# Optimization experiments

Hardware: AMD Instinct MI355X
Metric: run time of the kernel (lower is better)

## Reference

```python
import jax, jax.numpy as jnp
import numpy as np

D_K = 32
TOPK_FRAC = 0.1
DROP_P = 0.1


def setup_inputs() -> dict:
    key = jax.random.key(0)
    k1, k2, k3, k4 = jax.random.split(key, 4)
    B, F, N, T = 4, 64, 4096, 12
    dim = T * F  # 768
    x = jax.random.normal(k1, (B, F, N, T), dtype=jnp.float32)
    # nn.Linear(dim, d_k, bias=False): y = x @ W.T ; store W transposed as [dim, d_k]
    W_Q = jax.random.normal(k2, (dim, D_K), dtype=jnp.float32) * (1.0 / np.sqrt(dim))
    W_K = jax.random.normal(k3, (dim, D_K), dtype=jnp.float32) * (1.0 / np.sqrt(dim))
    # uniform noise driving F.dropout (training=True) deterministically
    drop_u = jax.random.uniform(k4, (N, N), dtype=jnp.float32)
    return {"x": x, "W_Q": W_Q, "W_K": W_K, "drop_u": drop_u}


def _drop(attn, drop_u):
    # k = int(N*N*0.1); topk over flattened matrix
    N, M = attn.shape
    k = int(N * M * TOPK_FRAC)
    flat = attn.reshape(-1)
    _, idx = jax.lax.top_k(flat, k)
    topk_mask = jnp.zeros_like(flat).at[idx].set(1.0).reshape(N, M)
    kept = attn * topk_mask
    # F.dropout on the remainder: zero with prob p, scale survivors by 1/(1-p)
    keep = (drop_u >= DROP_P).astype(attn.dtype)
    remaining = attn * (1.0 - topk_mask) * keep * (1.0 / (1.0 - DROP_P))
    return kept + remaining


def reference(x, W_Q, W_K, drop_u):
    B, F, N, T = x.shape
    # [B, F, N, T] -> [B, N, T, F] -> [B, N, T*F]
    xr = jnp.transpose(x, (0, 2, 3, 1)).reshape(B, N, T * F)
    Q = xr @ W_Q  # [B, N, d_k]
    K = xr @ W_K  # [B, N, d_k]
    scores = jnp.einsum("bnd,bmd->bnm", Q, K) * (1.0 / np.sqrt(D_K))  # [B, N, N]
    attn = jax.nn.softmax(jnp.sum(scores, axis=0), axis=-1)  # [N, N]
    return _drop(attn, drop_u)
```

## Files before the change

kernel.cpp:

```cpp
#include <hip/hip_runtime.h>
#include <stdint.h>

#define NN 4096
#define KSEL_S 419430u
#define INV_SQRT_DK 0.17677669529663687f

#define OFF_QH 0u
#define OFF_KH (1u<<20)
#define OFF_STATS (2u<<20)
#define OFF_H   (3u<<20)
#define OFF_H2  (4u<<20)
#define OFF_ST  ((4u<<20) + 65536u)
#define OFF_MASK (5u<<20)
#define OFF_SB  (16u<<20)
#define WS_NEED_B16 (48u<<20)

#define LDB 104

typedef __attribute__((ext_vector_type(8))) short bf16x8;
typedef __attribute__((ext_vector_type(8))) unsigned short u16x8;
typedef __attribute__((ext_vector_type(4))) float f32x4;

static __device__ __forceinline__ short f2bf(float f) {
    unsigned u = __float_as_uint(f);
    unsigned r = (u + 0x7FFFu + ((u >> 16) & 1u)) >> 16;
    return (short)r;
}
static __device__ __forceinline__ float bf2f(short h) {
    return __uint_as_float(((unsigned)(unsigned short)h) << 16);
}

__global__ __launch_bounds__(256) void projmask_kernel(
    const float* __restrict__ x, const float* __restrict__ WQ,
    const float* __restrict__ WK,
    short* __restrict__ Qh, short* __restrict__ Kh,
    const float4* __restrict__ u4, unsigned* __restrict__ maskw)
{
    __shared__ short Ah[2][64 * LDB];
    __shared__ short Al[2][64 * LDB];
    __shared__ short Bl[2][64 * LDB];
    const int bxg = blockIdx.x;
    const int tid = threadIdx.x;

    if (bxg >= 256) {
        const unsigned word = (unsigned)(bxg - 256) * 256 + tid;
        const float4* __restrict__ up = u4 + (size_t)word * 8;
        unsigned m = 0;
#pragma unroll
        for (int j = 0; j < 8; ++j) {
            float4 a = up[j];
            m |= (a.x >= 0.1f ? 1u : 0u) << (4 * j);
            m |= (a.y >= 0.1f ? 2u : 0u) << (4 * j);
            m |= (a.z >= 0.1f ? 4u : 0u) << (4 * j);
            m |= (a.w >= 0.1f ? 8u : 0u) << (4 * j);
        }
        maskw[word] = m;
        return;
    }

    const int bx  = bxg;
    const int b   = bx >> 6;
    const int n0  = (bx & 63) << 6;
    const int l   = tid & 63;
    const int w   = __builtin_amdgcn_readfirstlane(tid >> 6);
    const int lr  = l & 15;
    const int kg  = (l >> 4) * 8;

    f32x4 acc[4];
#pragma unroll
    for (int j = 0; j < 4; ++j) acc[j] = (f32x4){0.f, 0.f, 0.f, 0.f};

    auto STAGE = [&](int c, int sbuf) {
#pragma unroll
        for (int j = 0; j < 6; ++j) {
            const int s   = tid + (j << 8);
            const int f_l = s / 192;
            const int rem = s - f_l * 192;
            const int r   = rem / 3;
            const int t4  = rem - r * 3;
            float4 v = *(const float4*)(x + (size_t)b * 3145728
                                          + (size_t)(c * 8 + f_l) * 49152
                                          + (size_t)(n0 + r) * 12 + t4 * 4);
            const int kl = f_l * 12 + t4 * 4;
            short4 hi, lo;
            hi.x = f2bf(v.x); lo.x = f2bf(v.x - bf2f(hi.x));
            hi.y = f2bf(v.y); lo.y = f2bf(v.y - bf2f(hi.y));
            hi.z = f2bf(v.z); lo.z = f2bf(v.z - bf2f(hi.z));
            hi.w = f2bf(v.w); lo.w = f2bf(v.w - bf2f(hi.w));
            *(short4*)&Ah[sbuf][r * LDB + kl] = hi;
            *(short4*)&Al[sbuf][r * LDB + kl] = lo;
        }
#pragma unroll
        for (int j = 0; j < 6; ++j) {
            const int s   = tid + (j << 8);
            const int qk  = (s >= 768) ? 1 : 0;
            const int rem = s - qk * 768;
            const int kr  = rem >> 3;
            const int c4  = rem & 7;
            const int t   = kr % 12;
            const int f_l = kr / 12;
            const float* __restrict__ Wp = qk ? WK : WQ;
            float4 wv = *(const float4*)(Wp + (size_t)(t * 64 + c * 8 + f_l) * 32 + (c4 << 2));
            const int kl = f_l * 12 + t;
            const int col = (qk << 5) + (c4 << 2);
            Bl[sbuf][(col + 0) * LDB + kl] = f2bf(wv.x);
            Bl[sbuf][(col + 1) * LDB + kl] = f2bf(wv.y);
            Bl[sbuf][(col + 2) * LDB + kl] = f2bf(wv.z);
            Bl[sbuf][(col + 3) * LDB + kl] = f2bf(wv.w);
        }
    };

    STAGE(0, 0);
    int buf = 0;
    for (int c = 0; c < 8; ++c) {
        __syncthreads();
        if (c < 7) STAGE(c + 1, buf ^ 1);
#pragma unroll
        for (int ks = 0; ks < 3; ++ks) {
            const int ko = ks * 32 + kg;
            bf16x8 ah = *(const bf16x8*)&Ah[buf][(w * 16 + lr) * LDB + ko];
            bf16x8 al = *(const bf16x8*)&Al[buf][(w * 16 + lr) * LDB + ko];
#pragma unroll
            for (int j = 0; j < 4; ++j) {
                bf16x8 bb = *(const bf16x8*)&Bl[buf][(j * 16 + lr) * LDB + ko];
                acc[j] = __builtin_amdgcn_mfma_f32_16x16x32_bf16(ah, bb, acc[j], 0, 0, 0);
                acc[j] = __builtin_amdgcn_mfma_f32_16x16x32_bf16(al, bb, acc[j], 0, 0, 0);
            }
        }
        buf ^= 1;
    }

#pragma unroll
    for (int j = 0; j < 4; ++j) {
        const int col = j * 16 + lr;
#pragma unroll
        for (int r = 0; r < 4; ++r) {
            const int row = n0 + w * 16 + (l >> 4) * 4 + r;
            if (col < 32)
                Qh[(size_t)row * 128 + (b << 5) + col] = f2bf(acc[j][r] * INV_SQRT_DK);
            else
                Kh[(size_t)row * 128 + (b << 5) + (col - 32)] = f2bf(acc[j][r]);
        }
    }
}

template<bool B16>
__global__ __launch_bounds__(256, 3) void gemm_kernel(
    const short* __restrict__ Qh, const short* __restrict__ Kh, void* Sv)
{
    const int bi = blockIdx.x >> 5, bj = blockIdx.x & 31;
    const int tid = threadIdx.x;
    const int w = tid >> 6, l = tid & 63;
    const int m0 = bi * 128 + (w >> 1) * 64;
    const int n0 = bj * 128 + (w & 1) * 64;
    const int lr = l & 15;
    const int kg = (l >> 4) * 8;

    f32x4 acc[4][4];
#pragma unroll
    for (int i = 0; i < 4; ++i)
#pragma unroll
        for (int j = 0; j < 4; ++j) acc[i][j] = (f32x4){0.f, 0.f, 0.f, 0.f};

    bf16x8 aA[4], bA[4], aB[4], bB[4];

    auto LD = [&](bf16x8* A, bf16x8* B, int k0) {
#pragma unroll
        for (int i = 0; i < 4; ++i) {
            A[i] = *(const bf16x8*)(Qh + (size_t)(m0 + i * 16 + lr) * 128 + k0 + kg);
            B[i] = *(const bf16x8*)(Kh + (size_t)(n0 + i * 16 + lr) * 128 + k0 + kg);
        }
    };
    auto DOMFMA = [&](bf16x8* A, bf16x8* B) {
#pragma unroll
        for (int i = 0; i < 4; ++i)
#pragma unroll
            for (int j = 0; j < 4; ++j)
                acc[i][j] = __builtin_amdgcn_mfma_f32_16x16x32_bf16(A[i], B[j], acc[i][j], 0, 0, 0);
    };

    LD(aA, bA, 0);
    LD(aB, bB, 32);
    DOMFMA(aA, bA);  LD(aA, bA, 64);
    DOMFMA(aB, bB);  LD(aB, bB, 96);
    DOMFMA(aA, bA);
    DOMFMA(aB, bB);

#pragma unroll
    for (int i = 0; i < 4; ++i) {
        int rowb = m0 + i * 16 + (l >> 4) * 4;
#pragma unroll
        for (int j = 0; j < 4; ++j) {
            int col = n0 + j * 16 + (l & 15);
#pragma unroll
            for (int r = 0; r < 4; ++r) {
                if constexpr (B16)
                    ((unsigned short*)Sv)[(size_t)(rowb + r) * NN + col] =
                        (unsigned short)f2bf(acc[i][j][r]);
                else
                    ((float*)Sv)[(size_t)(rowb + r) * NN + col] = acc[i][j][r];
            }
        }
    }
}

template<bool B16>
__global__ __launch_bounds__(512) void histstat_kernel(
    const void* __restrict__ Sv, float2* __restrict__ stats,
    unsigned* __restrict__ gh)
{
    __shared__ unsigned h[1024];
    const int tid = threadIdx.x;
    const int l = tid & 63;
    const int w = tid >> 6;

    for (int i = tid; i < 1024; i += 512) h[i] = 0;
    __syncthreads();

#pragma unroll
    for (int r = 0; r < 2; ++r) {
        const int row = (blockIdx.x << 4) + (r << 3) + w;

        float v[64];
        if constexpr (B16) {
            const u16x8* rp = (const u16x8*)((const unsigned short*)Sv + (size_t)row * NN);
#pragma unroll
            for (int j = 0; j < 8; ++j) {
                u16x8 e = rp[l + (j << 6)];
#pragma unroll
                for (int i = 0; i < 8; ++i) v[j * 8 + i] = bf2f((short)e[i]);
            }
        } else {
            const float4* rp = (const float4*)((const float*)Sv + (size_t)row * NN);
#pragma unroll
            for (int j = 0; j < 16; ++j) {
                float4 t = rp[l + (j << 6)];
                v[j * 4 + 0] = t.x; v[j * 4 + 1] = t.y;
                v[j * 4 + 2] = t.z; v[j * 4 + 3] = t.w;
            }
        }

        float s = 0.f;
#pragma unroll
        for (int j = 0; j < 64; ++j) { v[j] = __expf(v[j]); s += v[j]; }
#pragma unroll
        for (int off = 32; off; off >>= 1) s += __shfl_xor(s, off);
        const float inv = 1.0f / s;
        if (l == 0) stats[row] = make_float2(0.f, inv);

        if constexpr (B16) {
#pragma unroll
            for (int jj = 0; jj < 2; ++jj) {
                const int base = jj * 32;
#pragma unroll
                for (int c = 0; c < 8; ++c) {
                    int b0 = min(max((int)(__float_as_uint(v[base + c] * inv) >> 16) - 0x3780, 0), 1023);
                    atomicAdd(&h[b0], 1u);
                }
            }
        } else {
#pragma unroll
            for (int jj = 0; jj < 4; ++jj) {
                const int base = jj * 16;
#pragma unroll
                for (int c = 0; c < 4; ++c) {
                    int b0 = min(max((int)(__float_as_uint(v[base + c] * inv) >> 16) - 0x3780, 0), 1023);
                    atomicAdd(&h[b0], 1u);
                }
            }
        }
    }

    __syncthreads();
    unsigned* dst = gh + ((unsigned)blockIdx.x << 10);
    for (int i = tid; i < 1024; i += 512) dst[i] = h[i];
}

__global__ __launch_bounds__(1024) void reduce_kernel(
    const unsigned* __restrict__ gh, unsigned* __restrict__ gh2)
{
    const int t = threadIdx.x, b = blockIdx.x;
    unsigned s = 0;
    for (int p = 0; p < 32; ++p) s += gh[((unsigned)(b * 32 + p) << 10) + t];
    gh2[((unsigned)b << 10) + t] = s;
}

__global__ __launch_bounds__(1024) void scan_kernel(
    const unsigned* __restrict__ gh2, unsigned* st)
{
    __shared__ unsigned P[1024];
    const int t = threadIdx.x;
    unsigned s = 0;
#pragma unroll
    for (int p = 0; p < 8; ++p) s += gh2[(p << 10) + t];
    P[t] = s;
    __syncthreads();
    for (int off = 1; off < 1024; off <<= 1) {
        unsigned v = P[t] + ((t + off < 1024) ? P[t + off] : 0u);
        __syncthreads();
        P[t] = v;
        __syncthreads();
    }
    if (P[t] >= KSEL_S && (t == 1023 || P[t + 1] < KSEL_S))
        st[2] = (0x3780u + (unsigned)t) << 16;
}

template<bool B16>
__global__ __launch_bounds__(256) void final_kernel(
    const void* __restrict__ Sv, float* __restrict__ out,
    const unsigned* __restrict__ maskw,
    const float2* __restrict__ stats, const unsigned* __restrict__ st)
{
    const int row = blockIdx.x;
    const int tid = threadIdx.x;
    const float thr = __uint_as_float(st[2]);
    const float2 stt = stats[row];
    float4* o4 = (float4*)(out + (size_t)row * NN);
    const unsigned* mw = maskw + (size_t)row * 128;

    float4 sv[4];
    unsigned wv[4];

    if constexpr (B16) {
        const ushort4* S4 = (const ushort4*)((const unsigned short*)Sv + (size_t)row * NN);
        ushort4 sraw[4];
#pragma unroll
        for (int j = 0; j < 4; ++j) sraw[j] = S4[tid + (j << 8)];
#pragma unroll
        for (int j = 0; j < 4; ++j) wv[j] = mw[(tid >> 3) + (j << 5)];
#pragma unroll
        for (int j = 0; j < 4; ++j) {
            sv[j].x = bf2f((short)sraw[j].x); sv[j].y = bf2f((short)sraw[j].y);
            sv[j].z = bf2f((short)sraw[j].z); sv[j].w = bf2f((short)sraw[j].w);
        }
    } else {
        const float4* S4 = (const float4*)((const float*)Sv + (size_t)row * NN);
#pragma unroll
        for (int j = 0; j < 4; ++j) sv[j] = S4[tid + (j << 8)];
#pragma unroll
        for (int j = 0; j < 4; ++j) wv[j] = mw[(tid >> 3) + (j << 5)];
    }

    const unsigned sh = (tid & 7) << 2;
#pragma unroll
    for (int j = 0; j < 4; ++j) {
        const unsigned bits = (wv[j] >> sh) & 0xFu;
        float4 o;
        float p;
        p = __expf(sv[j].x - stt.x) * stt.y;
        o.x = (p >= thr) ? p : ((bits & 1u) ? p * (1.0f / 0.9f) : 0.0f);
        p = __expf(sv[j].y - stt.x) * stt.y;
        o.y = (p >= thr) ? p : ((bits & 2u) ? p * (1.0f / 0.9f) : 0.0f);
        p = __expf(sv[j].z - stt.x) * stt.y;
        o.z = (p >= thr) ? p : ((bits & 4u) ? p * (1.0f / 0.9f) : 0.0f);
        p = __expf(sv[j].w - stt.x) * stt.y;
        o.w = (p >= thr) ? p : ((bits & 8u) ? p * (1.0f / 0.9f) : 0.0f);
        o4[tid + (j << 8)] = o;
    }
}

extern "C" void kernel_launch(void* const* d_in, const int* in_sizes, int n_in,
                              void* d_out, int out_size, void* d_ws, size_t ws_size,
                              hipStream_t stream)
{
    const float* x  = (const float*)d_in[0];
    const float* WQ = (const float*)d_in[1];
    const float* WK = (const float*)d_in[2];
    const float* du = (const float*)d_in[3];
    float* out = (float*)d_out;
    char* ws = (char*)d_ws;

    short* Qh = (short*)(ws + OFF_QH);
    short* Kh = (short*)(ws + OFF_KH);
    float2* stats = (float2*)(ws + OFF_STATS);
    unsigned* hist = (unsigned*)(ws + OFF_H);
    unsigned* gh2  = (unsigned*)(ws + OFF_H2);
    unsigned* st   = (unsigned*)(ws + OFF_ST);
    unsigned* mask = (unsigned*)(ws + OFF_MASK);

    projmask_kernel<<<2304, 256, 0, stream>>>(x, WQ, WK, Qh, Kh,
                                              (const float4*)du, mask);

    const bool b16 = (ws_size >= (size_t)WS_NEED_B16);
    if (b16) {
        void* Sb = (void*)(ws + OFF_SB);
        gemm_kernel<true><<<1024, 256, 0, stream>>>(Qh, Kh, Sb);
        histstat_kernel<true><<<256, 512, 0, stream>>>(Sb, stats, hist);
        reduce_kernel<<<8, 1024, 0, stream>>>(hist, gh2);
        scan_kernel<<<1, 1024, 0, stream>>>(gh2, st);
        final_kernel<true><<<NN, 256, 0, stream>>>(Sb, out, mask, stats, st);
    } else {
        gemm_kernel<false><<<1024, 256, 0, stream>>>(Qh, Kh, (void*)out);
        histstat_kernel<false><<<256, 512, 0, stream>>>((void*)out, stats, hist);
        reduce_kernel<<<8, 1024, 0, stream>>>(hist, gh2);
        scan_kernel<<<1, 1024, 0, stream>>>(gh2, st);
        final_kernel<false><<<NN, 256, 0, stream>>>((void*)out, out, mask, stats, st);
    }
}
```

Baseline: 80.61 us.

## Fuse dropout-mask packing into projection blocks as extra waves

Instead of launching 2048 separate blocks to pack the dropout keep-mask, each projection block gets 256 extra threads that pack the mask in chunks alongside the bf16 projection GEMM. The intent is to overlap the bandwidth-bound read of the uniform noise with the compute-bound projection. Loads are also made coalesced, with consecutive threads reading consecutive float4s and nibbles combined via xor-shuffles. The mask threads join the projection loop's barriers, and the projection loop is marked not to unroll. The risk is that only 256 blocks with 4 mask waves each may not issue enough memory traffic to saturate HBM.

```diff
diff --git a/kernel.cpp b/kernel.cpp
--- a/kernel.cpp
+++ b/kernel.cpp
@@ -30,7 +30,7 @@
     return __uint_as_float(((unsigned)(unsigned short)h) << 16);
 }
 
-__global__ __launch_bounds__(256) void projmask_kernel(
+__global__ __launch_bounds__(512) void projmask_kernel(
     const float* __restrict__ x, const float* __restrict__ WQ,
     const float* __restrict__ WK,
     short* __restrict__ Qh, short* __restrict__ Kh,
@@ -39,26 +39,32 @@
     __shared__ short Ah[2][64 * LDB];
     __shared__ short Al[2][64 * LDB];
     __shared__ short Bl[2][64 * LDB];
-    const int bxg = blockIdx.x;
+    const int bx  = blockIdx.x;
     const int tid = threadIdx.x;
 
-    if (bxg >= 256) {
-        const unsigned word = (unsigned)(bxg - 256) * 256 + tid;
-        const float4* __restrict__ up = u4 + (size_t)word * 8;
-        unsigned m = 0;
-#pragma unroll
-        for (int j = 0; j < 8; ++j) {
-            float4 a = up[j];
-            m |= (a.x >= 0.1f ? 1u : 0u) << (4 * j);
-            m |= (a.y >= 0.1f ? 2u : 0u) << (4 * j);
-            m |= (a.z >= 0.1f ? 4u : 0u) << (4 * j);
-            m |= (a.w >= 0.1f ? 8u : 0u) << (4 * j);
-        }
-        maskw[word] = m;
+    if (tid >= 256) {
+        const int mt = tid - 256;
+        const int l8 = mt & 7;
+#pragma unroll 1
+        for (int c = 0; c < 8; ++c) {
+            __syncthreads();
+            const unsigned f4base = ((unsigned)bx << 14) + ((unsigned)c << 11);
+#pragma unroll
+            for (int j = 0; j < 8; ++j) {
+                const unsigned idx = f4base + (unsigned)(j << 8) + (unsigned)mt;
+                float4 a = u4[idx];
+                unsigned nib = (a.x >= 0.1f ? 1u : 0u) | (a.y >= 0.1f ? 2u : 0u)
+                             | (a.z >= 0.1f ? 4u : 0u) | (a.w >= 0.1f ? 8u : 0u);
+                unsigned v = nib << (4 * l8);
+                v |= (unsigned)__shfl_xor((int)v, 1);
+                v |= (unsigned)__shfl_xor((int)v, 2);
+                v |= (unsigned)__shfl_xor((int)v, 4);
+                if (l8 == 0) maskw[idx >> 3] = v;
+            }
+        }
         return;
     }
 
-    const int bx  = bxg;
     const int b   = bx >> 6;
     const int n0  = (bx & 63) << 6;
     const int l   = tid & 63;
@@ -112,6 +118,7 @@
 
     STAGE(0, 0);
     int buf = 0;
+#pragma unroll 1
     for (int c = 0; c < 8; ++c) {
         __syncthreads();
         if (c < 7) STAGE(c + 1, buf ^ 1);
@@ -378,8 +385,8 @@
     unsigned* st   = (unsigned*)(ws + OFF_ST);
     unsigned* mask = (unsigned*)(ws + OFF_MASK);
 
-    projmask_kernel<<<2304, 256, 0, stream>>>(x, WQ, WK, Qh, Kh,
-                                              (const float4*)du, mask);
+    projmask_kernel<<<256, 512, 0, stream>>>(x, WQ, WK, Qh, Kh,
+                                             (const float4*)du, mask);
 
     const bool b16 = (ws_size >= (size_t)WS_NEED_B16);
     if (b16) {
```

After: 88.84 us. 10.2% more time.
